# Optimization experiments

Hardware: AMD Instinct MI355X
Metric: run time of the kernel (lower is better)

Reference implementation:

```python
import jax, jax.numpy as jnp
import numpy as np

N = 100000
E = 1600000
D_IN = 128
HID = 128
LN_EPS = 1e-5
GIN_EPS = 0.0  # PyG GINConv default eps


def setup_inputs() -> dict:
    key = jax.random.key(0)
    ks = jax.random.split(key, 8)
    x = jax.random.normal(ks[0], (N, D_IN), dtype=jnp.float32)
    edge_index = jax.random.randint(ks[1], (2, E), 0, N, dtype=jnp.int64)
    s1 = 1.0 / np.sqrt(D_IN)
    s2 = 1.0 / np.sqrt(HID)
    W1 = jax.random.uniform(ks[2], (D_IN, HID), jnp.float32, -s1, s1)
    b1 = jnp.zeros((HID,), jnp.float32)
    W2 = jax.random.uniform(ks[3], (HID, HID), jnp.float32, -s2, s2)
    b2 = jnp.zeros((HID,), jnp.float32)
    gamma = jnp.ones((HID,), jnp.float32)
    beta = jnp.zeros((HID,), jnp.float32)
    Wres = jax.random.uniform(ks[4], (D_IN, HID), jnp.float32, -s1, s1)
    bres = jnp.zeros((HID,), jnp.float32)
    return {"x": x, "edge_index": edge_index, "W1": W1, "b1": b1,
            "W2": W2, "b2": b2, "gamma": gamma, "beta": beta,
            "Wres": Wres, "bres": bres}


def reference(x, edge_index, W1, b1, W2, b2, gamma, beta, Wres, bres):
    src, dst = edge_index[0], edge_index[1]
    # GIN sum aggregation: scatter-add source features onto targets. [N, D_IN]
    agg = jax.ops.segment_sum(x[src], dst, num_segments=N)
    h = (1.0 + GIN_EPS) * x + agg
    # GIN MLP: Linear -> ReLU -> Linear
    h = jax.nn.relu(h @ W1 + b1) @ W2 + b2
    # LayerNorm over hidden dim
    mu = jnp.mean(h, axis=-1, keepdims=True)
    var = jnp.mean(jnp.square(h - mu), axis=-1, keepdims=True)
    h = (h - mu) * jax.lax.rsqrt(var + LN_EPS) * gamma + beta
    # dropout p=0 is identity; residual linear path
    return h + (x @ Wres + bres)
```

## Files before the change

### kernel.cpp

```cpp
#include <hip/hip_runtime.h>

#define NN 100000
#define NE 1600000
#define D 128
#define RT 64
#define NB 196
#define CAP 9216
#define PADB 136

typedef unsigned short u16;
typedef __attribute__((ext_vector_type(8))) short bf16x8;
typedef __attribute__((ext_vector_type(4))) float f32x4;

__device__ __forceinline__ u16 f2bf(float f) {
  unsigned int u = __float_as_uint(f);
  u += 0x7fffu + ((u >> 16) & 1u);
  return (u16)(u >> 16);
}

__global__ __launch_bounds__(256) void prep_kernel(const float* __restrict__ x,
                                                   const float* __restrict__ W1,
                                                   const float* __restrict__ W2,
                                                   const float* __restrict__ Wres,
                                                   u16* __restrict__ xh,
                                                   u16* __restrict__ wt,
                                                   int* __restrict__ tail) {
  int b = blockIdx.x;
  int t = threadIdx.x;
  if (b < 12500) {
    int q = b * 256 + t;
    float4 v = ((const float4*)x)[q];
    uint2 pk;
    pk.x = (unsigned)f2bf(v.x) | ((unsigned)f2bf(v.y) << 16);
    pk.y = (unsigned)f2bf(v.z) | ((unsigned)f2bf(v.w) << 16);
    ((uint2*)xh)[q] = pk;
  } else if (b < 12503) {
    const float* W = (b == 12500) ? Wres : (b == 12501) ? W1 : W2;
    u16* dst = wt + (size_t)(b - 12500) * 16384;
    for (int i = t; i < 16384; i += 256) {
      int n = i >> 7, k = i & 127;
      dst[i] = f2bf(W[k * 128 + n]);
    }
  } else {
    tail[t] = 0;
  }
}

__global__ __launch_bounds__(512) void bucket_kernel(const int* __restrict__ ei,
                                                     int* __restrict__ tail,
                                                     unsigned* __restrict__ buf) {
  __shared__ int lhist[NB], lbase[NB];
  int t = threadIdx.x;
  size_t e0 = (size_t)blockIdx.x * 8192;
  int s[16], d[16];
  for (int j = t; j < NB; j += 512) lhist[j] = 0;
  __syncthreads();
#pragma unroll
  for (int k = 0; k < 16; ++k) {
    size_t e = e0 + t + (size_t)k * 512;
    if (e < NE) {
      d[k] = ei[NE + e];
      s[k] = ei[e];
      atomicAdd(&lhist[d[k] >> 9], 1);
    } else {
      d[k] = -1;
    }
  }
  __syncthreads();
  for (int j = t; j < NB; j += 512) {
    int c = lhist[j];
    lbase[j] = c ? atomicAdd(&tail[j], c) : 0;
    lhist[j] = 0;
  }
  __syncthreads();
#pragma unroll
  for (int k = 0; k < 16; ++k) {
    if (d[k] >= 0) {
      int bk = d[k] >> 9;
      int r = lbase[bk] + atomicAdd(&lhist[bk], 1);
      if (r < CAP)
        buf[(size_t)bk * CAP + r] = (unsigned)s[k] | ((unsigned)(d[k] & 511) << 17);
    }
  }
}

__global__ __launch_bounds__(512) void build_csr(const unsigned* __restrict__ buf,
                                                 const int* __restrict__ tail,
                                                 int* __restrict__ cnt,
                                                 int* __restrict__ start,
                                                 int* __restrict__ csr) {
  __shared__ int lhist[512], lpre[512], lsum[64];
  int b = blockIdx.x, t = threadIdx.x;
  int nE = tail[b];
  if (nE > CAP) nE = CAP;
  size_t bBase = (size_t)b * CAP;
  lhist[t] = 0;
  __syncthreads();
  for (int i = t; i < nE; i += 512)
    atomicAdd(&lhist[buf[bBase + i] >> 17], 1);
  __syncthreads();
  if (t < 64) {
    int s = 0;
#pragma unroll
    for (int k = 0; k < 8; ++k) { int v = lhist[t * 8 + k]; lpre[t * 8 + k] = s; s += v; }
    lsum[t] = s;
  }
  __syncthreads();
  if (t == 0) {
    int s = 0;
    for (int k = 0; k < 64; ++k) { int v = lsum[k]; lsum[k] = s; s += v; }
  }
  __syncthreads();
  if (t < 64) {
    int o = lsum[t];
#pragma unroll
    for (int k = 0; k < 8; ++k) lpre[t * 8 + k] += o;
  }
  __syncthreads();
  int node = (b << 9) + t;
  if (node < NN) {
    cnt[node] = lhist[t];
    start[node] = (int)bBase + lpre[t];
  }
  lhist[t] = 0;
  __syncthreads();
  for (int i = t; i < nE; i += 512) {
    unsigned e = buf[bBase + i];
    int dl = e >> 17;
    int r = atomicAdd(&lhist[dl], 1);
    csr[bBase + lpre[dl] + r] = (int)(e & 0x1FFFFu);
  }
}

#define BFACC(a, v)                                        \
  { a.x += __uint_as_float((v).x << 16);                   \
    a.y += __uint_as_float((v).x & 0xffff0000u);           \
    a.z += __uint_as_float((v).y << 16);                   \
    a.w += __uint_as_float((v).y & 0xffff0000u); }

__global__ __launch_bounds__(256, 8) void gather_kernel(const float* __restrict__ x,
                                                        const u16* __restrict__ xh,
                                                        const int* __restrict__ cnt,
                                                        const int* __restrict__ start,
                                                        const int* __restrict__ csr,
                                                        float* __restrict__ h0) {
  int g = blockIdx.x * 8 + (threadIdx.x >> 5);
  if (g >= NN) return;
  int lane = threadIdx.x & 31;
  int fo = lane * 4;
  int n = cnt[g];
  const int* sp = csr + start[g];

  float4 a0 = make_float4(0.f, 0.f, 0.f, 0.f);
  float4 a1 = a0, a2 = a0, a3 = a0;

  int nfull = n & ~3;
  if (nfull > 0) {
    int s0 = sp[0], s1 = sp[1], s2 = sp[2], s3 = sp[3];
    uint2 v0 = *(const uint2*)&xh[(size_t)s0 * D + fo];
    uint2 v1 = *(const uint2*)&xh[(size_t)s1 * D + fo];
    uint2 v2 = *(const uint2*)&xh[(size_t)s2 * D + fo];
    uint2 v3 = *(const uint2*)&xh[(size_t)s3 * D + fo];
#pragma unroll 2
    for (int j = 4; j < nfull; j += 4) {
      int t0 = sp[j], t1 = sp[j + 1], t2 = sp[j + 2], t3 = sp[j + 3];
      uint2 w0 = *(const uint2*)&xh[(size_t)t0 * D + fo];
      uint2 w1 = *(const uint2*)&xh[(size_t)t1 * D + fo];
      uint2 w2 = *(const uint2*)&xh[(size_t)t2 * D + fo];
      uint2 w3 = *(const uint2*)&xh[(size_t)t3 * D + fo];
      BFACC(a0, v0); BFACC(a1, v1); BFACC(a2, v2); BFACC(a3, v3);
      v0 = w0; v1 = w1; v2 = w2; v3 = w3;
    }
    BFACC(a0, v0); BFACC(a1, v1); BFACC(a2, v2); BFACC(a3, v3);
  }
  for (int j = nfull; j < n; ++j) {
    int s0 = sp[j];
    uint2 v0 = *(const uint2*)&xh[(size_t)s0 * D + fo];
    BFACC(a0, v0);
  }

  float4 xv = *(const float4*)&x[(size_t)g * D + fo];
  float4 r;
  r.x = xv.x + (a0.x + a1.x) + (a2.x + a3.x);
  r.y = xv.y + (a0.y + a1.y) + (a2.y + a3.y);
  r.z = xv.z + (a0.z + a1.z) + (a2.z + a3.z);
  r.w = xv.w + (a0.w + a1.w) + (a2.w + a3.w);
  *(float4*)&h0[(size_t)g * D + fo] = r;
}

__global__ __launch_bounds__(256, 3) void fused_kernel(
    const u16* __restrict__ xh, const float* __restrict__ h0,
    const u16* __restrict__ wt,
    const float* __restrict__ b1, const float* __restrict__ b2,
    const float* __restrict__ gamma, const float* __restrict__ beta,
    const float* __restrict__ bres, float* __restrict__ out) {
  __shared__ u16 As[RT * PADB];

  const int t = threadIdx.x;
  const int w = t >> 6;
  const int lane = t & 63;
  const int quad = lane >> 4;
  const int l16 = lane & 15;
  const int row0 = blockIdx.x * RT;

  auto stage_bf = [&](const u16* __restrict__ src) {
#pragma unroll
    for (int i = 0; i < 8; ++i) {
      int v = t + i * 256;
      int r = v >> 5;
      int c4 = (v & 31) << 2;
      int row = row0 + r;
      uint2 val = make_uint2(0u, 0u);
      if (row < NN) val = *(const uint2*)&src[(size_t)row * D + c4];
      *(uint2*)&As[r * PADB + c4] = val;
    }
  };
  auto stage_f32 = [&](const float* __restrict__ src) {
#pragma unroll
    for (int i = 0; i < 8; ++i) {
      int v = t + i * 256;
      int r = v >> 5;
      int c4 = (v & 31) << 2;
      int row = row0 + r;
      uint2 pk = make_uint2(0u, 0u);
      if (row < NN) {
        float4 f = *(const float4*)&src[(size_t)row * D + c4];
        pk.x = (unsigned)f2bf(f.x) | ((unsigned)f2bf(f.y) << 16);
        pk.y = (unsigned)f2bf(f.z) | ((unsigned)f2bf(f.w) << 16);
      }
      *(uint2*)&As[r * PADB + c4] = pk;
    }
  };

  f32x4 acc[8], accR[8];
  f32x4 zz = {0.f, 0.f, 0.f, 0.f};
#pragma unroll
  for (int i = 0; i < 8; ++i) { acc[i] = zz; accR[i] = zz; }

  auto gemm = [&](const u16* __restrict__ W, f32x4 (&dd)[8]) {
    bf16x8 af[4];
#pragma unroll
    for (int s = 0; s < 4; ++s)
      af[s] = *(const bf16x8*)&As[(w * 16 + l16) * PADB + s * 32 + quad * 8];
#pragma unroll
    for (int nt = 0; nt < 8; ++nt) {
      const u16* wp = W + (size_t)(nt * 16 + l16) * D + quad * 8;
#pragma unroll
      for (int s = 0; s < 4; ++s) {
        bf16x8 bf = *(const bf16x8*)&wp[s * 32];
        dd[nt] = __builtin_amdgcn_mfma_f32_16x16x32_bf16(af[s], bf, dd[nt], 0, 0, 0);
      }
    }
  };

  stage_bf(xh);
  __syncthreads();
  gemm(wt, accR);
  __syncthreads();

  stage_f32(h0);
  __syncthreads();
  gemm(wt + 16384, acc);
  __syncthreads();

#pragma unroll
  for (int nt = 0; nt < 8; ++nt) {
    int col = nt * 16 + l16;
    float bb = b1[col];
#pragma unroll
    for (int r = 0; r < 4; ++r) {
      float hv = acc[nt][r] + bb;
      hv = hv > 0.f ? hv : 0.f;
      As[(w * 16 + quad * 4 + r) * PADB + col] = f2bf(hv);
      acc[nt][r] = 0.f;
    }
  }
  __syncthreads();
  gemm(wt + 32768, acc);

  float b2v[8], gv[8], bev[8], brv[8];
#pragma unroll
  for (int nt = 0; nt < 8; ++nt) {
    int col = nt * 16 + l16;
    b2v[nt] = b2[col];
    gv[nt] = gamma[col];
    bev[nt] = beta[col];
    brv[nt] = bres[col];
  }
#pragma unroll
  for (int r = 0; r < 4; ++r) {
    float s = 0.f, s2 = 0.f;
#pragma unroll
    for (int nt = 0; nt < 8; ++nt) {
      float h = acc[nt][r] + b2v[nt];
      s += h;
      s2 += h * h;
    }
    for (int m = 1; m <= 8; m <<= 1) {
      s += __shfl_xor(s, m);
      s2 += __shfl_xor(s2, m);
    }
    float mu = s * 0.0078125f;
    float var = s2 * 0.0078125f - mu * mu;
    float rs = rsqrtf(var + 1e-5f);
    int row = row0 + w * 16 + quad * 4 + r;
    if (row < NN) {
#pragma unroll
      for (int nt = 0; nt < 8; ++nt) {
        float h = acc[nt][r] + b2v[nt];
        out[(size_t)row * D + nt * 16 + l16] =
            (h - mu) * rs * gv[nt] + bev[nt] + accR[nt][r] + brv[nt];
      }
    }
  }
}

extern "C" void kernel_launch(void* const* d_in, const int* in_sizes, int n_in,
                              void* d_out, int out_size, void* d_ws, size_t ws_size,
                              hipStream_t stream) {
  const float* x     = (const float*)d_in[0];
  const int*   ei    = (const int*)d_in[1];
  const float* W1    = (const float*)d_in[2];
  const float* b1    = (const float*)d_in[3];
  const float* W2    = (const float*)d_in[4];
  const float* b2    = (const float*)d_in[5];
  const float* gamma = (const float*)d_in[6];
  const float* beta  = (const float*)d_in[7];
  const float* Wres  = (const float*)d_in[8];
  const float* bres  = (const float*)d_in[9];
  float* out = (float*)d_out;

  int*      tail  = (int*)d_ws;
  unsigned* buf   = (unsigned*)(tail + 256);
  int*      cnt   = (int*)(buf + (size_t)NB * CAP);
  int*      start = cnt + NN;
  int*      csr   = start + NN;
  u16*      xh    = (u16*)(csr + (size_t)NB * CAP);
  u16*      wt    = xh + (size_t)NN * D;

  float* h0 = out;

  prep_kernel<<<12504, 256, 0, stream>>>(x, W1, W2, Wres, xh, wt, tail);
  bucket_kernel<<<196, 512, 0, stream>>>(ei, tail, buf);
  build_csr<<<NB, 512, 0, stream>>>(buf, tail, cnt, start, csr);
  gather_kernel<<<(NN + 7) / 8, 256, 0, stream>>>(x, xh, cnt, start, csr, h0);
  fused_kernel<<<(NN + RT - 1) / RT, 256, 0, stream>>>(
      xh, h0, wt, b1, b2, gamma, beta, bres, out);
}
```

Baseline: 316.5 us.

## Fuse neighbor gather into the MLP kernel, writing aggregated rows straight to LDS

Removes the separate gather kernel. Each fused block now aggregates neighbor features for its 64 rows and writes the result as bf16 into shared memory, so the fp32 intermediate h0 is no longer written to and re-read from global memory. The residual GEMM now loads its xh A-fragments directly from global memory instead of staging them in LDS, and the occupancy hint rises from 3 to 4 blocks. The trade-off is fewer independent warps doing irregular gathers, since each block has only 8 warps serially covering 64 rows. This may reduce latency hiding compared with the dedicated high-occupancy gather kernel.

```diff
diff --git a/kernel.cpp b/kernel.cpp
--- a/kernel.cpp
+++ b/kernel.cpp
@@ -138,63 +138,14 @@
     a.z += __uint_as_float((v).y << 16);                   \
     a.w += __uint_as_float((v).y & 0xffff0000u); }
 
-__global__ __launch_bounds__(256, 8) void gather_kernel(const float* __restrict__ x,
-                                                        const u16* __restrict__ xh,
-                                                        const int* __restrict__ cnt,
-                                                        const int* __restrict__ start,
-                                                        const int* __restrict__ csr,
-                                                        float* __restrict__ h0) {
-  int g = blockIdx.x * 8 + (threadIdx.x >> 5);
-  if (g >= NN) return;
-  int lane = threadIdx.x & 31;
-  int fo = lane * 4;
-  int n = cnt[g];
-  const int* sp = csr + start[g];
-
-  float4 a0 = make_float4(0.f, 0.f, 0.f, 0.f);
-  float4 a1 = a0, a2 = a0, a3 = a0;
-
-  int nfull = n & ~3;
-  if (nfull > 0) {
-    int s0 = sp[0], s1 = sp[1], s2 = sp[2], s3 = sp[3];
-    uint2 v0 = *(const uint2*)&xh[(size_t)s0 * D + fo];
-    uint2 v1 = *(const uint2*)&xh[(size_t)s1 * D + fo];
-    uint2 v2 = *(const uint2*)&xh[(size_t)s2 * D + fo];
-    uint2 v3 = *(const uint2*)&xh[(size_t)s3 * D + fo];
-#pragma unroll 2
-    for (int j = 4; j < nfull; j += 4) {
-      int t0 = sp[j], t1 = sp[j + 1], t2 = sp[j + 2], t3 = sp[j + 3];
-      uint2 w0 = *(const uint2*)&xh[(size_t)t0 * D + fo];
-      uint2 w1 = *(const uint2*)&xh[(size_t)t1 * D + fo];
-      uint2 w2 = *(const uint2*)&xh[(size_t)t2 * D + fo];
-      uint2 w3 = *(const uint2*)&xh[(size_t)t3 * D + fo];
-      BFACC(a0, v0); BFACC(a1, v1); BFACC(a2, v2); BFACC(a3, v3);
-      v0 = w0; v1 = w1; v2 = w2; v3 = w3;
-    }
-    BFACC(a0, v0); BFACC(a1, v1); BFACC(a2, v2); BFACC(a3, v3);
-  }
-  for (int j = nfull; j < n; ++j) {
-    int s0 = sp[j];
-    uint2 v0 = *(const uint2*)&xh[(size_t)s0 * D + fo];
-    BFACC(a0, v0);
-  }
-
-  float4 xv = *(const float4*)&x[(size_t)g * D + fo];
-  float4 r;
-  r.x = xv.x + (a0.x + a1.x) + (a2.x + a3.x);
-  r.y = xv.y + (a0.y + a1.y) + (a2.y + a3.y);
-  r.z = xv.z + (a0.z + a1.z) + (a2.z + a3.z);
-  r.w = xv.w + (a0.w + a1.w) + (a2.w + a3.w);
-  *(float4*)&h0[(size_t)g * D + fo] = r;
-}
-
-__global__ __launch_bounds__(256, 3) void fused_kernel(
-    const u16* __restrict__ xh, const float* __restrict__ h0,
-    const u16* __restrict__ wt,
+__global__ __launch_bounds__(256, 4) void fused_kernel(
+    const float* __restrict__ x, const u16* __restrict__ xh,
+    const int* __restrict__ cnt, const int* __restrict__ start,
+    const int* __restrict__ csr, const u16* __restrict__ wt,
     const float* __restrict__ b1, const float* __restrict__ b2,
     const float* __restrict__ gamma, const float* __restrict__ beta,
     const float* __restrict__ bres, float* __restrict__ out) {
-  __shared__ u16 As[RT * PADB];
+  __shared__ u16 Hs[RT * PADB];
 
   const int t = threadIdx.x;
   const int w = t >> 6;
@@ -203,45 +154,65 @@
   const int l16 = lane & 15;
   const int row0 = blockIdx.x * RT;
 
-  auto stage_bf = [&](const u16* __restrict__ src) {
-#pragma unroll
-    for (int i = 0; i < 8; ++i) {
-      int v = t + i * 256;
-      int r = v >> 5;
-      int c4 = (v & 31) << 2;
-      int row = row0 + r;
-      uint2 val = make_uint2(0u, 0u);
-      if (row < NN) val = *(const uint2*)&src[(size_t)row * D + c4];
-      *(uint2*)&As[r * PADB + c4] = val;
-    }
-  };
-  auto stage_f32 = [&](const float* __restrict__ src) {
-#pragma unroll
-    for (int i = 0; i < 8; ++i) {
-      int v = t + i * 256;
-      int r = v >> 5;
-      int c4 = (v & 31) << 2;
-      int row = row0 + r;
+  {
+    const int lane32 = t & 31;
+    const int rloc = t >> 5;
+    const int fo = lane32 * 4;
+    for (int pass = 0; pass < 8; ++pass) {
+      int r = pass * 8 + rloc;
+      int g = row0 + r;
       uint2 pk = make_uint2(0u, 0u);
-      if (row < NN) {
-        float4 f = *(const float4*)&src[(size_t)row * D + c4];
-        pk.x = (unsigned)f2bf(f.x) | ((unsigned)f2bf(f.y) << 16);
-        pk.y = (unsigned)f2bf(f.z) | ((unsigned)f2bf(f.w) << 16);
+      if (g < NN) {
+        int n = cnt[g];
+        const int* sp = csr + start[g];
+        float4 a0 = make_float4(0.f, 0.f, 0.f, 0.f);
+        float4 a1 = a0, a2 = a0, a3 = a0;
+        int nfull = n & ~3;
+        if (nfull > 0) {
+          int s0 = sp[0], s1 = sp[1], s2 = sp[2], s3 = sp[3];
+          uint2 v0 = *(const uint2*)&xh[(size_t)s0 * D + fo];
+          uint2 v1 = *(const uint2*)&xh[(size_t)s1 * D + fo];
+          uint2 v2 = *(const uint2*)&xh[(size_t)s2 * D + fo];
+          uint2 v3 = *(const uint2*)&xh[(size_t)s3 * D + fo];
+#pragma unroll 2
+          for (int j = 4; j < nfull; j += 4) {
+            int t0 = sp[j], t1 = sp[j + 1], t2 = sp[j + 2], t3 = sp[j + 3];
+            uint2 w0 = *(const uint2*)&xh[(size_t)t0 * D + fo];
+            uint2 w1 = *(const uint2*)&xh[(size_t)t1 * D + fo];
+            uint2 w2 = *(const uint2*)&xh[(size_t)t2 * D + fo];
+            uint2 w3 = *(const uint2*)&xh[(size_t)t3 * D + fo];
+            BFACC(a0, v0); BFACC(a1, v1); BFACC(a2, v2); BFACC(a3, v3);
+            v0 = w0; v1 = w1; v2 = w2; v3 = w3;
+          }
+          BFACC(a0, v0); BFACC(a1, v1); BFACC(a2, v2); BFACC(a3, v3);
+        }
+        for (int j = nfull; j < n; ++j) {
+          int s0 = sp[j];
+          uint2 v0 = *(const uint2*)&xh[(size_t)s0 * D + fo];
+          BFACC(a0, v0);
+        }
+        float4 xv = *(const float4*)&x[(size_t)g * D + fo];
+        float hx = xv.x + (a0.x + a1.x) + (a2.x + a3.x);
+        float hy = xv.y + (a0.y + a1.y) + (a2.y + a3.y);
+        float hz = xv.z + (a0.z + a1.z) + (a2.z + a3.z);
+        float hw = xv.w + (a0.w + a1.w) + (a2.w + a3.w);
+        pk.x = (unsigned)f2bf(hx) | ((unsigned)f2bf(hy) << 16);
+        pk.y = (unsigned)f2bf(hz) | ((unsigned)f2bf(hw) << 16);
       }
-      *(uint2*)&As[r * PADB + c4] = pk;
-    }
-  };
+      *(uint2*)&Hs[r * PADB + fo] = pk;
+    }
+  }
 
   f32x4 acc[8], accR[8];
   f32x4 zz = {0.f, 0.f, 0.f, 0.f};
 #pragma unroll
   for (int i = 0; i < 8; ++i) { acc[i] = zz; accR[i] = zz; }
 
-  auto gemm = [&](const u16* __restrict__ W, f32x4 (&dd)[8]) {
+  auto gemmL = [&](const u16* __restrict__ W, f32x4 (&dd)[8]) {
     bf16x8 af[4];
 #pragma unroll
     for (int s = 0; s < 4; ++s)
-      af[s] = *(const bf16x8*)&As[(w * 16 + l16) * PADB + s * 32 + quad * 8];
+      af[s] = *(const bf16x8*)&Hs[(w * 16 + l16) * PADB + s * 32 + quad * 8];
 #pragma unroll
     for (int nt = 0; nt < 8; ++nt) {
       const u16* wp = W + (size_t)(nt * 16 + l16) * D + quad * 8;
@@ -252,15 +223,26 @@
       }
     }
   };
-
-  stage_bf(xh);
-  __syncthreads();
-  gemm(wt, accR);
-  __syncthreads();
-
-  stage_f32(h0);
-  __syncthreads();
-  gemm(wt + 16384, acc);
+  auto gemmG = [&](const u16* __restrict__ A, const u16* __restrict__ W,
+                   f32x4 (&dd)[8]) {
+    bf16x8 af[4];
+#pragma unroll
+    for (int s = 0; s < 4; ++s)
+      af[s] = *(const bf16x8*)&A[(size_t)(row0 + w * 16 + l16) * D + s * 32 + quad * 8];
+#pragma unroll
+    for (int nt = 0; nt < 8; ++nt) {
+      const u16* wp = W + (size_t)(nt * 16 + l16) * D + quad * 8;
+#pragma unroll
+      for (int s = 0; s < 4; ++s) {
+        bf16x8 bf = *(const bf16x8*)&wp[s * 32];
+        dd[nt] = __builtin_amdgcn_mfma_f32_16x16x32_bf16(af[s], bf, dd[nt], 0, 0, 0);
+      }
+    }
+  };
+
+  __syncthreads();
+  gemmG(xh, wt, accR);
+  gemmL(wt + 16384, acc);
   __syncthreads();
 
 #pragma unroll
@@ -271,12 +253,12 @@
     for (int r = 0; r < 4; ++r) {
       float hv = acc[nt][r] + bb;
       hv = hv > 0.f ? hv : 0.f;
-      As[(w * 16 + quad * 4 + r) * PADB + col] = f2bf(hv);
+      Hs[(w * 16 + quad * 4 + r) * PADB + col] = f2bf(hv);
       acc[nt][r] = 0.f;
     }
   }
   __syncthreads();
-  gemm(wt + 32768, acc);
+  gemmL(wt + 32768, acc);
 
   float b2v[8], gv[8], bev[8], brv[8];
 #pragma unroll
@@ -338,12 +320,9 @@
   u16*      xh    = (u16*)(csr + (size_t)NB * CAP);
   u16*      wt    = xh + (size_t)NN * D;
 
-  float* h0 = out;
-
   prep_kernel<<<12504, 256, 0, stream>>>(x, W1, W2, Wres, xh, wt, tail);
   bucket_kernel<<<196, 512, 0, stream>>>(ei, tail, buf);
   build_csr<<<NB, 512, 0, stream>>>(buf, tail, cnt, start, csr);
-  gather_kernel<<<(NN + 7) / 8, 256, 0, stream>>>(x, xh, cnt, start, csr, h0);
   fused_kernel<<<(NN + RT - 1) / RT, 256, 0, stream>>>(
-      xh, h0, wt, b1, b2, gamma, beta, bres, out);
-}
+      x, xh, cnt, start, csr, wt, b1, b2, gamma, beta, bres, out);
+}
```

After: 335.9 us. 6.1% more time.
